# Kernel optimization log

Hardware: AMD Instinct MI355X
Metric: run time of the kernel (lower is better)

## Reference

```python
import jax, jax.numpy as jnp
import numpy as np

NEG_INF = -1e30  # stand-in for float('-inf') that stays nan-free under softmax


def setup_inputs() -> dict:
    key = jax.random.key(0)
    k0, k1, k2, k3 = jax.random.split(key, 4)
    B, T, E, H = 4, 2048, 1024, 64
    X = jax.random.normal(k0, (B, T, E), dtype=jnp.float32)
    Wq = jax.random.normal(k1, (E, H), dtype=jnp.float32) * (E ** -0.5)
    Wk = jax.random.normal(k2, (E, H), dtype=jnp.float32) * (E ** -0.5)
    Wv = jax.random.normal(k3, (E, H), dtype=jnp.float32) * (E ** -0.5)
    return {"X": X, "Wq": Wq, "Wk": Wk, "Wv": Wv}


def reference(X, Wq, Wk, Wv):
    # X: [B, T, E]; W*: [E, H]
    B, T, C = X.shape
    Q = jnp.einsum('bte,eh->bth', X, Wq)
    K = jnp.einsum('bte,eh->bth', X, Wk)
    V = jnp.einsum('bte,eh->bth', X, Wv)
    # NOTE: original scales by emb_size**-0.5 (C), not head_size**-0.5
    wei = jnp.einsum('bqh,bkh->bqk', Q, K) * (C ** -0.5)  # [B, T, T]
    causal = jnp.tril(jnp.ones((T, T), dtype=bool))
    wei = jnp.where(causal, wei, NEG_INF)
    wei = jax.nn.softmax(wei, axis=-1)
    # dropout rate = 0.0 (eval-mode equivalent) -> identity
    out = jnp.einsum('bqk,bkh->bqh', wei, V)  # [B, T, H]
    return out
```

## Files before the change

### kernel.cpp

```cpp
#include <hip/hip_runtime.h>
#include <hip/hip_bf16.h>

constexpr int Bc = 4;
constexpr int Tc = 2048;
constexpr int Ec = 1024;
constexpr int Hc = 64;
constexpr float SCALE = 0.03125f;

typedef short  short8  __attribute__((ext_vector_type(8)));
typedef float  floatx4 __attribute__((ext_vector_type(4)));

__device__ __forceinline__ unsigned short f2bf(float f) {
    union { float f; unsigned int i; } x;
    x.f = f;
    unsigned int r = x.i + 0x7fffu + ((x.i >> 16) & 1u);
    return (unsigned short)(r >> 16);
}

__global__ __launch_bounds__(256) void prep_w(
    const float* __restrict__ Wq, const float* __restrict__ Wk,
    const float* __restrict__ Wv, unsigned short* __restrict__ Wt)
{
    const float* W = blockIdx.y == 0 ? Wq : (blockIdx.y == 1 ? Wk : Wv);
    unsigned short* D = Wt + (size_t)blockIdx.y * (Ec * Hc);
    const int i0 = blockIdx.x * 1024 + threadIdx.x * 4;
    const float4 f = *(const float4*)(W + i0);
    const float v[4] = {f.x, f.y, f.z, f.w};
    #pragma unroll
    for (int j = 0; j < 4; ++j) {
        const int i = i0 + j;
        D[(i & 63) * Ec + (i >> 6)] = f2bf(v[j]);
    }
}

__global__ __launch_bounds__(256) void qkv_mfma10(
    const float* __restrict__ X, const unsigned short* __restrict__ Wt,
    unsigned short* __restrict__ Q, unsigned short* __restrict__ K,
    unsigned short* __restrict__ Vt)
{
    __shared__ __align__(16) unsigned short Xs[16][136];
    __shared__ __align__(16) unsigned short Ws[3][64][128];

    const int tid  = threadIdx.x;
    const int wv   = tid >> 6;
    const int lane = tid & 63;
    const int quad = lane >> 4;
    const int l16  = lane & 15;
    const size_t row0 = (size_t)blockIdx.x * 16;

    floatx4 acc[3];
    #pragma unroll
    for (int j = 0; j < 3; ++j)
        #pragma unroll
        for (int r = 0; r < 4; ++r) acc[j][r] = 0.f;

    const int xrow = tid >> 4;
    const int xc4  = (tid & 15) * 4;


    for (int k0 = 0; k0 < Ec; k0 += 128) {
        __syncthreads();
        #pragma unroll
        for (int h = 0; h < 2; ++h) {
            const float4 f = *(const float4*)(X + (row0 + xrow) * Ec + k0 + h * 64 + xc4);
            uint2 p;
            p.x = (unsigned int)f2bf(f.x) | ((unsigned int)f2bf(f.y) << 16);
            p.y = (unsigned int)f2bf(f.z) | ((unsigned int)f2bf(f.w) << 16);
            *(uint2*)&Xs[xrow][h * 64 + xc4] = p;
        }
        #pragma unroll
        for (int j = 0; j < 12; ++j) {
            const int flat  = tid + 256 * j;
            const int which = flat >> 10;
            const int r     = (flat >> 4) & 63;
            const int chunk = (flat & 15) ^ (r & 7);
            const unsigned short* src = Wt + which * 65536 + r * 1024 + k0 + chunk * 8;
            char* dst = (char*)&Ws[0][0][0] + (wv * 64 + 256 * j) * 16;
            __builtin_amdgcn_global_load_lds(
                (const __attribute__((address_space(1))) unsigned int*)src,
                (__attribute__((address_space(3))) unsigned int*)dst,
                16, 0, 0);
        }
        __syncthreads();

        #pragma unroll
        for (int ks = 0; ks < 4; ++ks) {
            const short8 a = *(const short8*)&Xs[l16][ks * 32 + quad * 8];
            short8 b[3];
            #pragma unroll
            for (int j = 0; j < 3; ++j) {
                const int f    = 3 * wv + j;
                const int row  = 16 * (f & 3) + l16;
                const int colb = (ks * 64 + quad * 16) ^ ((l16 & 7) << 4);
                b[j] = *(const short8*)((const char*)&Ws[f >> 2][row][0] + colb);
            }
            #pragma unroll
            for (int j = 0; j < 3; ++j)
                acc[j] = __builtin_amdgcn_mfma_f32_16x16x32_bf16(a, b[j], acc[j], 0, 0, 0);
        }
    }

    #pragma unroll
    for (int j = 0; j < 3; ++j) {
        const int f  = 3 * wv + j;
        const int mf = f >> 2, nf = f & 3;
        if (mf < 2) {
            unsigned short* O = mf == 0 ? Q : K;
            #pragma unroll
            for (int r = 0; r < 4; ++r) {
                float x = acc[j][r];
                if (!(x > -1.0e4f && x < 1.0e4f)) x = 11111.0f;
                O[(row0 + quad * 4 + r) * Hc + 16 * nf + l16] = f2bf(x);
            }
        } else {
            const size_t b  = row0 >> 11;
            const int    t0 = (int)(row0 & 2047) + quad * 4;
            unsigned short* VtB = Vt + b * ((size_t)Hc * Tc);
            unsigned int pk[2];
            #pragma unroll
            for (int half = 0; half < 2; ++half) {
                float x0 = acc[j][half * 2 + 0], x1 = acc[j][half * 2 + 1];
                if (!(x0 > -1.0e4f && x0 < 1.0e4f)) x0 = 11111.0f;
                if (!(x1 > -1.0e4f && x1 < 1.0e4f)) x1 = 11111.0f;
                pk[half] = (unsigned int)f2bf(x0) | ((unsigned int)f2bf(x1) << 16);
            }
            uint2 st; st.x = pk[0]; st.y = pk[1];
            *(uint2*)(VtB + (size_t)(16 * nf + l16) * Tc + t0) = st;
        }
    }
}

__global__ __launch_bounds__(512, 4) void attn_mfma6(
    const unsigned short* __restrict__ Q, const unsigned short* __restrict__ K,
    const unsigned short* __restrict__ Vt, float* __restrict__ Out)
{
    __shared__ __align__(16) unsigned short Pb[8][16][72];
    __shared__ __align__(16) float accS[8][16][64];
    __shared__ __align__(16) float lSr[8][16];

    const int tid  = threadIdx.x;
    const int wv   = tid >> 6;
    const int lane = tid & 63;
    const int quad = lane >> 4;
    const int l16  = lane & 15;
    const int id   = blockIdx.x + 128 * blockIdx.y;
    const int jj   = id & 255;
    const int qt   = (id < 256) ? (127 - (jj >> 2)) : (jj >> 2);
    const int b    = jj & 3;
    const int qend = qt * 16 + 16;
    const size_t base = (size_t)b * Tc * Hc;
    const unsigned short* VtB = Vt + (size_t)b * Hc * Tc;

    short8 aQ[2];
    #pragma unroll
    for (int ks = 0; ks < 2; ++ks)
        aQ[ks] = *(const short8*)(Q + base +
            (size_t)(qt * 16 + l16) * Hc + ks * 32 + quad * 8);

    floatx4 acc[4];
    float l_st[4];
    #pragma unroll
    for (int nh = 0; nh < 4; ++nh)
        #pragma unroll
        for (int r = 0; r < 4; ++r) acc[nh][r] = 0.f;
    #pragma unroll
    for (int r = 0; r < 4; ++r) l_st[r] = 0.f;

    for (int kb = wv * 64; kb < qend; kb += 512) {
        floatx4 s[4];
        #pragma unroll
        for (int ni = 0; ni < 4; ++ni)
            #pragma unroll
            for (int r = 0; r < 4; ++r) s[ni][r] = 0.f;
        #pragma unroll
        for (int ks = 0; ks < 2; ++ks) {
            short8 bk[4];
            #pragma unroll
            for (int ni = 0; ni < 4; ++ni)
                bk[ni] = *(const short8*)(K + base +
                    (size_t)(kb + 16 * ni + l16) * Hc + ks * 32 + quad * 8);
            __builtin_amdgcn_s_setprio(1);
            #pragma unroll
            for (int ni = 0; ni < 4; ++ni)
                s[ni] = __builtin_amdgcn_mfma_f32_16x16x32_bf16(aQ[ks], bk[ni], s[ni], 0, 0, 0);
            __builtin_amdgcn_s_setprio(0);
        }

        #pragma unroll
        for (int r = 0; r < 4; ++r) {
            const int qrow = qt * 16 + quad * 4 + r;
            #pragma unroll
            for (int ni = 0; ni < 4; ++ni) {
                const int kcol = kb + 16 * ni + l16;
                const float p = (kcol > qrow) ? 0.f : __expf(s[ni][r] * SCALE);
                s[ni][r] = p;
                l_st[r] += p;
            }
        }
        #pragma unroll
        for (int ni = 0; ni < 4; ++ni)
            #pragma unroll
            for (int r = 0; r < 4; ++r)
                Pb[wv][quad * 4 + r][16 * ni + l16] = f2bf(s[ni][r]);

        #pragma unroll
        for (int ks = 0; ks < 2; ++ks) {
            const short8 aP = *(const short8*)&Pb[wv][l16][ks * 32 + quad * 8];
            short8 bv[4];
            #pragma unroll
            for (int nh = 0; nh < 4; ++nh)
                bv[nh] = *(const short8*)(VtB +
                    (size_t)(16 * nh + l16) * Tc + kb + ks * 32 + quad * 8);
            __builtin_amdgcn_s_setprio(1);
            #pragma unroll
            for (int nh = 0; nh < 4; ++nh)
                acc[nh] = __builtin_amdgcn_mfma_f32_16x16x32_bf16(aP, bv[nh], acc[nh], 0, 0, 0);
            __builtin_amdgcn_s_setprio(0);
        }
    }

    #pragma unroll
    for (int nh = 0; nh < 4; ++nh)
        #pragma unroll
        for (int r = 0; r < 4; ++r)
            accS[wv][quad * 4 + r][16 * nh + l16] = acc[nh][r];
    #pragma unroll
    for (int r = 0; r < 4; ++r) {
        float v = l_st[r];
        v += __shfl_xor(v, 1);
        v += __shfl_xor(v, 2);
        v += __shfl_xor(v, 4);
        v += __shfl_xor(v, 8);
        l_st[r] = v;
    }
    if (l16 == 0)
        #pragma unroll
        for (int r = 0; r < 4; ++r)
            lSr[wv][quad * 4 + r] = l_st[r];
    __syncthreads();

    {
        const int q  = tid >> 5;
        const int h0 = (tid & 31) * 2;
        float denom = 0.f;
        #pragma unroll
        for (int w = 0; w < 8; ++w)
            denom += lSr[w][q];
        const float inv = 1.f / denom;
        float o0 = 0.f, o1 = 0.f;
        #pragma unroll
        for (int w = 0; w < 8; ++w) {
            const float2 v = *(const float2*)&accS[w][q][h0];
            o0 += v.x; o1 += v.y;
        }
        o0 *= inv; o1 *= inv;
        if (!(o0 > -1.0e5f && o0 < 1.0e5f)) o0 = 555.0f;
        if (!(o1 > -1.0e5f && o1 < 1.0e5f)) o1 = 555.0f;
        float2 st; st.x = o0; st.y = o1;
        *(float2*)(Out + base + (size_t)(qt * 16 + q) * Hc + h0) = st;
    }
}

extern "C" void kernel_launch(void* const* d_in, const int* in_sizes, int n_in,
                              void* d_out, int out_size, void* d_ws, size_t ws_size,
                              hipStream_t stream)
{
    const float* X  = (const float*)d_in[0];
    const float* Wq = (const float*)d_in[1];
    const float* Wk = (const float*)d_in[2];
    const float* Wv = (const float*)d_in[3];

    const size_t N = (size_t)Bc * Tc * Hc;
    unsigned short* Wt  = (unsigned short*)d_ws;
    unsigned short* Qws = Wt + 3 * (size_t)Ec * Hc;
    unsigned short* Kws = Qws + N;
    unsigned short* Vtw = Kws + N;

    prep_w<<<dim3(64, 3), dim3(256), 0, stream>>>(Wq, Wk, Wv, Wt);
    qkv_mfma10<<<dim3(512), dim3(256), 0, stream>>>(X, Wt, Qws, Kws, Vtw);
    attn_mfma6<<<dim3(128, 4), dim3(512), 0, stream>>>(
        Qws, Kws, Vtw, (float*)d_out);
}
```

Before: 108.1 us.

## Double-buffer QKV projection with register-prefetched X and packed bf16 conversion

```diff
diff --git a/kernel.cpp b/kernel.cpp
--- a/kernel.cpp
+++ b/kernel.cpp
@@ -15,6 +15,12 @@
     x.f = f;
     unsigned int r = x.i + 0x7fffu + ((x.i >> 16) & 1u);
     return (unsigned short)(r >> 16);
+}
+
+__device__ __forceinline__ unsigned int cvt_pk_bf16(float lo, float hi) {
+    unsigned int r;
+    asm volatile("v_cvt_pk_bf16_f32 %0, %1, %2" : "=v"(r) : "v"(lo), "v"(hi));
+    return r;
 }
 
 __global__ __launch_bounds__(256) void prep_w(
@@ -33,20 +39,21 @@
     }
 }
 
-__global__ __launch_bounds__(256) void qkv_mfma10(
+__global__ __launch_bounds__(512, 2) void qkv_mfma12(
     const float* __restrict__ X, const unsigned short* __restrict__ Wt,
     unsigned short* __restrict__ Q, unsigned short* __restrict__ K,
     unsigned short* __restrict__ Vt)
 {
-    __shared__ __align__(16) unsigned short Xs[16][136];
-    __shared__ __align__(16) unsigned short Ws[3][64][128];
+    __shared__ __align__(16) unsigned short Ws[2][3][64][128];
 
     const int tid  = threadIdx.x;
     const int wv   = tid >> 6;
     const int lane = tid & 63;
     const int quad = lane >> 4;
     const int l16  = lane & 15;
-    const size_t row0 = (size_t)blockIdx.x * 16;
+    const int rowh = wv >> 2;
+    const int wq   = wv & 3;
+    const size_t row0 = (size_t)blockIdx.x * 32;
 
     floatx4 acc[3];
     #pragma unroll
@@ -54,55 +61,94 @@
         #pragma unroll
         for (int r = 0; r < 4; ++r) acc[j][r] = 0.f;
 
-    const int xrow = tid >> 4;
-    const int xc4  = (tid & 15) * 4;
-
-
-    for (int k0 = 0; k0 < Ec; k0 += 128) {
-        __syncthreads();
-        #pragma unroll
-        for (int h = 0; h < 2; ++h) {
-            const float4 f = *(const float4*)(X + (row0 + xrow) * Ec + k0 + h * 64 + xc4);
-            uint2 p;
-            p.x = (unsigned int)f2bf(f.x) | ((unsigned int)f2bf(f.y) << 16);
-            p.y = (unsigned int)f2bf(f.z) | ((unsigned int)f2bf(f.w) << 16);
-            *(uint2*)&Xs[xrow][h * 64 + xc4] = p;
-        }
-        #pragma unroll
-        for (int j = 0; j < 12; ++j) {
-            const int flat  = tid + 256 * j;
-            const int which = flat >> 10;
-            const int r     = (flat >> 4) & 63;
-            const int chunk = (flat & 15) ^ (r & 7);
-            const unsigned short* src = Wt + which * 65536 + r * 1024 + k0 + chunk * 8;
-            char* dst = (char*)&Ws[0][0][0] + (wv * 64 + 256 * j) * 16;
-            __builtin_amdgcn_global_load_lds(
-                (const __attribute__((address_space(1))) unsigned int*)src,
-                (__attribute__((address_space(3))) unsigned int*)dst,
-                16, 0, 0);
-        }
-        __syncthreads();
-
-        #pragma unroll
-        for (int ks = 0; ks < 4; ++ks) {
-            const short8 a = *(const short8*)&Xs[l16][ks * 32 + quad * 8];
-            short8 b[3];
-            #pragma unroll
-            for (int j = 0; j < 3; ++j) {
-                const int f    = 3 * wv + j;
-                const int row  = 16 * (f & 3) + l16;
-                const int colb = (ks * 64 + quad * 16) ^ ((l16 & 7) << 4);
-                b[j] = *(const short8*)((const char*)&Ws[f >> 2][row][0] + colb);
-            }
-            #pragma unroll
-            for (int j = 0; j < 3; ++j)
-                acc[j] = __builtin_amdgcn_mfma_f32_16x16x32_bf16(a, b[j], acc[j], 0, 0, 0);
-        }
-    }
-
+    const float* Xrow = X + (row0 + rowh * 16 + l16) * Ec + quad * 8;
+
+    float4 xA[8], xB[8];
+
+    #pragma unroll
+    for (int j = 0; j < 6; ++j) {
+        const int flat  = tid + 512 * j;
+        const int which = flat >> 10;
+        const int r     = (flat >> 4) & 63;
+        const int chunk = (flat & 15) ^ (r & 7);
+        const unsigned short* src = Wt + which * 65536 + r * 1024 + chunk * 8;
+        char* dst = (char*)&Ws[0][0][0][0] + (wv * 64 + 512 * j) * 16;
+        __builtin_amdgcn_global_load_lds(
+            (const __attribute__((address_space(1))) unsigned int*)src,
+            (__attribute__((address_space(3))) unsigned int*)dst,
+            16, 0, 0);
+    }
+    #pragma unroll
+    for (int i = 0; i < 8; ++i)
+        xA[i] = *(const float4*)(Xrow + (i >> 1) * 32 + (i & 1) * 4);
+    __builtin_amdgcn_sched_barrier(0);
+    asm volatile("s_waitcnt vmcnt(8)" ::: "memory");
+    __builtin_amdgcn_s_barrier();
+
+#define QKV_STEP(T, CUR, XC, XN)                                              \
+    do {                                                                      \
+        if ((T) < 7) {                                                        \
+            const int k1 = ((T) + 1) * 128;                                   \
+            _Pragma("unroll")                                                 \
+            for (int j = 0; j < 6; ++j) {                                     \
+                const int flat  = tid + 512 * j;                              \
+                const int which = flat >> 10;                                 \
+                const int r     = (flat >> 4) & 63;                           \
+                const int chunk = (flat & 15) ^ (r & 7);                      \
+                const unsigned short* src =                                   \
+                    Wt + which * 65536 + r * 1024 + k1 + chunk * 8;           \
+                char* dst = (char*)&Ws[(CUR) ^ 1][0][0][0] +                  \
+                            (wv * 64 + 512 * j) * 16;                         \
+                __builtin_amdgcn_global_load_lds(                             \
+                    (const __attribute__((address_space(1))) unsigned int*)src,\
+                    (__attribute__((address_space(3))) unsigned int*)dst,     \
+                    16, 0, 0);                                                \
+            }                                                                 \
+            _Pragma("unroll")                                                 \
+            for (int i = 0; i < 8; ++i)                                       \
+                XN[i] = *(const float4*)(Xrow + k1 + (i >> 1) * 32 +          \
+                                         (i & 1) * 4);                        \
+        }                                                                     \
+        __builtin_amdgcn_sched_barrier(0);                                    \
+        _Pragma("unroll")                                                     \
+        for (int ks = 0; ks < 4; ++ks) {                                      \
+            union { unsigned int u[4]; short8 s8; } au;                       \
+            au.u[0] = cvt_pk_bf16(XC[ks * 2].x, XC[ks * 2].y);                \
+            au.u[1] = cvt_pk_bf16(XC[ks * 2].z, XC[ks * 2].w);                \
+            au.u[2] = cvt_pk_bf16(XC[ks * 2 + 1].x, XC[ks * 2 + 1].y);        \
+            au.u[3] = cvt_pk_bf16(XC[ks * 2 + 1].z, XC[ks * 2 + 1].w);        \
+            const short8 a = au.s8;                                           \
+            short8 b[3];                                                      \
+            _Pragma("unroll")                                                 \
+            for (int j = 0; j < 3; ++j) {                                     \
+                const int f    = 3 * wq + j;                                  \
+                const int row  = 16 * (f & 3) + l16;                          \
+                const int colb = (ks * 64 + quad * 16) ^ ((l16 & 7) << 4);    \
+                b[j] = *(const short8*)((const char*)&Ws[CUR][f >> 2][row][0] \
+                                        + colb);                              \
+            }                                                                 \
+            _Pragma("unroll")                                                 \
+            for (int j = 0; j < 3; ++j)                                       \
+                acc[j] = __builtin_amdgcn_mfma_f32_16x16x32_bf16(             \
+                    a, b[j], acc[j], 0, 0, 0);                                \
+        }                                                                     \
+        if ((T) < 7) {                                                        \
+            __builtin_amdgcn_sched_barrier(0);                                \
+            asm volatile("s_waitcnt vmcnt(8)" ::: "memory");                  \
+            __builtin_amdgcn_s_barrier();                                     \
+        }                                                                     \
+    } while (0)
+
+    for (int tt = 0; tt < 4; ++tt) {
+        QKV_STEP(2 * tt,     0, xA, xB);
+        QKV_STEP(2 * tt + 1, 1, xB, xA);
+    }
+#undef QKV_STEP
+
+    const size_t rbase = row0 + rowh * 16;
     #pragma unroll
     for (int j = 0; j < 3; ++j) {
-        const int f  = 3 * wv + j;
+        const int f  = 3 * wq + j;
         const int mf = f >> 2, nf = f & 3;
         if (mf < 2) {
             unsigned short* O = mf == 0 ? Q : K;
@@ -110,11 +156,11 @@
             for (int r = 0; r < 4; ++r) {
                 float x = acc[j][r];
                 if (!(x > -1.0e4f && x < 1.0e4f)) x = 11111.0f;
-                O[(row0 + quad * 4 + r) * Hc + 16 * nf + l16] = f2bf(x);
+                O[(rbase + quad * 4 + r) * Hc + 16 * nf + l16] = f2bf(x);
             }
         } else {
-            const size_t b  = row0 >> 11;
-            const int    t0 = (int)(row0 & 2047) + quad * 4;
+            const size_t b  = rbase >> 11;
+            const int    t0 = (int)(rbase & 2047) + quad * 4;
             unsigned short* VtB = Vt + b * ((size_t)Hc * Tc);
             unsigned int pk[2];
             #pragma unroll
@@ -130,7 +176,7 @@
     }
 }
 
-__global__ __launch_bounds__(512, 4) void attn_mfma6(
+__global__ __launch_bounds__(512, 4) void attn_mfma7(
     const unsigned short* __restrict__ Q, const unsigned short* __restrict__ K,
     const unsigned short* __restrict__ Vt, float* __restrict__ Out)
 {
@@ -198,10 +244,14 @@
             }
         }
         #pragma unroll
-        for (int ni = 0; ni < 4; ++ni)
-            #pragma unroll
-            for (int r = 0; r < 4; ++r)
-                Pb[wv][quad * 4 + r][16 * ni + l16] = f2bf(s[ni][r]);
+        for (int ni = 0; ni < 4; ++ni) {
+            const unsigned int a01 = cvt_pk_bf16(s[ni][0], s[ni][1]);
+            const unsigned int a23 = cvt_pk_bf16(s[ni][2], s[ni][3]);
+            Pb[wv][quad * 4 + 0][16 * ni + l16] = (unsigned short)a01;
+            Pb[wv][quad * 4 + 1][16 * ni + l16] = (unsigned short)(a01 >> 16);
+            Pb[wv][quad * 4 + 2][16 * ni + l16] = (unsigned short)a23;
+            Pb[wv][quad * 4 + 3][16 * ni + l16] = (unsigned short)(a23 >> 16);
+        }
 
         #pragma unroll
         for (int ks = 0; ks < 2; ++ks) {
@@ -277,7 +327,7 @@
     unsigned short* Vtw = Kws + N;
 
     prep_w<<<dim3(64, 3), dim3(256), 0, stream>>>(Wq, Wk, Wv, Wt);
-    qkv_mfma10<<<dim3(512), dim3(256), 0, stream>>>(X, Wt, Qws, Kws, Vtw);
-    attn_mfma6<<<dim3(128, 4), dim3(512), 0, stream>>>(
+    qkv_mfma12<<<dim3(256), dim3(512), 0, stream>>>(X, Wt, Qws, Kws, Vtw);
+    attn_mfma7<<<dim3(128, 4), dim3(512), 0, stream>>>(
         Qws, Kws, Vtw, (float*)d_out);
 }
```

Result: slower. 114.1 us (+5.5%).
